# Kernel tuning notes

Measured on AMD Instinct MI355X. Metric: run time of the kernel, lower is better.

Reference implementation:

```python
import jax, jax.numpy as jnp
import numpy as np


def _encode(tab, idx):
    # tab: [F, V, D]; idx: [..., F] int -> sum_f tab[f, idx[..., f]] -> [..., D]
    g = jax.vmap(lambda t, i: t[i], in_axes=(0, -1), out_axes=0)(tab, idx)
    return g.sum(0)


def _diffuse(fea, ei, w, order):
    # fea: [N, D]; ei: [2, E]; w: [E] learned edge weights
    N = fea.shape[0]
    r, c = ei[0], ei[1]
    adj = jnp.zeros((N, N), fea.dtype).at[r, c].set(w).at[c, r].set(w)
    adj = adj + jnp.eye(N, dtype=fea.dtype)
    r_col_inv = adj.sum(1) ** -0.5  # from degree over axis 1
    r_row_inv = adj.sum(0) ** -0.5  # from degree over axis 0
    A = r_row_inv[:, None] * adj * r_col_inv[None, :]
    x = fea
    y = fea
    for _ in range(order):
        x = jax.lax.stop_gradient(A @ x)
        y = y + x
    return jax.lax.stop_gradient(y / (order + 1.0))


def setup_inputs():
    B, N, E, EMB, L, FA, FB, V = 512, 128, 512, 300, 5, 9, 3, 64
    k = jax.random.split(jax.random.key(0), 12)
    s = 0.02
    return {
        "order": 3,
        "x_atom": jax.random.randint(k[0], (B, N, FA), 0, V),
        "edge_index": jax.random.randint(k[1], (B, 2, E), 0, N),
        "edge_attr": jax.random.randint(k[2], (B, E, FB), 0, V),
        "atom_tab": jax.random.normal(k[3], (FA, V, EMB)) * s,
        "bond_tab_root": jax.random.normal(k[4], (FB, V, EMB)) * s,
        "edge_lin_w": jax.random.normal(k[5], (EMB,)) * s,
        "edge_lin_b": jnp.zeros(()),
        "bond_tabs": jax.random.normal(k[6], (L, FB, V, EMB)) * s,
        "eps": jnp.zeros((L,)),
        "w1": jax.random.normal(k[7], (L, EMB, 2 * EMB)) * s,
        "b1": jnp.zeros((L, 2 * EMB)),
        "bn1_g": jnp.ones((L, 2 * EMB)),
        "bn1_b": jnp.zeros((L, 2 * EMB)),
        "w2": jax.random.normal(k[8], (L, 2 * EMB, EMB)) * s,
        "b2": jnp.zeros((L, EMB)),
        "bn_g": jnp.ones((L, EMB)),
        "bn_b": jnp.zeros((L, EMB)),
    }


def reference(order, x_atom, edge_index, edge_attr, atom_tab, bond_tab_root,
              edge_lin_w, edge_lin_b, bond_tabs, eps, w1, b1, bn1_g, bn1_b,
              w2, b2, bn_g, bn_b):
    B, N = x_atom.shape[:2]
    E = edge_index.shape[-1]
    L = w1.shape[0]
    DROP = 0.2  # node-feature drop rate (eval-mode scaling)

    # --- per-graph dense-adjacency diffusion (vmapped over graphs) ---
    fea = _encode(atom_tab, x_atom) * (1.0 - DROP)                 # [B, N, D]
    e_emb = _encode(bond_tab_root, edge_attr)                      # [B, E, D]
    ew = jax.nn.sigmoid(e_emb @ edge_lin_w + edge_lin_b)           # [B, E]
    h = jax.vmap(_diffuse, in_axes=(0, 0, 0, None))(fea, edge_index, ew, order)
    h = h.reshape(B * N, -1)                                       # [B*N, D]

    # --- globally-batched GIN message passing ---
    off = (jnp.arange(B) * N)[:, None]
    src = (edge_index[:, 0, :] + off).reshape(-1)                  # [B*E]
    dst = (edge_index[:, 1, :] + off).reshape(-1)
    ea_flat = edge_attr.reshape(B * E, -1)

    for l in range(L):
        ee = _encode(bond_tabs[l], ea_flat)                        # [B*E, D]
        msg = jax.nn.relu(h[src] + ee)
        agg = jax.ops.segment_sum(msg, dst, num_segments=B * N)
        z = (1.0 + eps[l]) * h + agg
        z = z @ w1[l] + b1[l]
        z = bn1_g[l] * z + bn1_b[l]   # eval-mode BN (running mean 0, var 1)
        z = jax.nn.relu(z)
        z = z @ w2[l] + b2[l]
        z = bn_g[l] * z + bn_b[l]     # outer eval-mode BN
        if l < L - 1:
            z = jax.nn.relu(z)
        h = z
    return h
```

## Files before the change

kernel.cpp:

```cpp
#include <hip/hip_runtime.h>

#define NGRAPH 512
#define NNODE  128
#define NEDGE  512
#define EMB    300
#define NLAYER 5
#define FA     9
#define FB     3
#define VV     64
#define KPAD   136

typedef __bf16 bf16x8 __attribute__((ext_vector_type(8)));
typedef __bf16 bf16x4 __attribute__((ext_vector_type(4)));
typedef float  f32x4  __attribute__((ext_vector_type(4)));

__device__ __forceinline__ void gload_lds16(const void* gptr, void* lptr) {
    __builtin_amdgcn_global_load_lds(
        (const __attribute__((address_space(1))) void*)gptr,
        (__attribute__((address_space(3))) void*)lptr, 16, 0, 0);
}

__global__ __launch_bounds__(256)
void prep_w_kernel(const float* __restrict__ w1, const float* __restrict__ w2,
                   __bf16* __restrict__ w1t, __bf16* __restrict__ w2t)
{
    const int i = blockIdx.x * 256 + threadIdx.x;
    const int T1 = NLAYER * 640 * 320;
    const int T2 = NLAYER * 320 * 640;
    if (i < T1) {
        const int l = i / (640 * 320);
        const int r = i - l * 640 * 320;
        const int n = r / 320, k = r - n * 320;
        float v = (n < 600 && k < 300) ? w1[((size_t)l * 300 + k) * 600 + n] : 0.f;
        w1t[i] = (__bf16)v;
    } else if (i < T1 + T2) {
        const int j = i - T1;
        const int l = j / (320 * 640);
        const int r = j - l * 320 * 640;
        const int n = r / 640, k = r - n * 640;
        float v = (n < 300 && k < 600) ? w2[((size_t)l * 600 + k) * 300 + n] : 0.f;
        w2t[j] = (__bf16)v;
    }
}

__global__ __launch_bounds__(128)
void csr_kernel(const int* __restrict__ edge_index,
                const int* __restrict__ edge_attr,
                int* __restrict__ epk_sorted,
                int* __restrict__ off_g)
{
    __shared__ int epk_s[NEDGE];
    __shared__ int cnt[128];
    __shared__ int off_[129];

    const int tid = threadIdx.x;
    const int g   = blockIdx.x;

    cnt[tid] = 0;
    __syncthreads();
    for (int e = tid; e < NEDGE; e += 128) {
        const int s_ = edge_index[(g * 2 + 0) * NEDGE + e];
        const int d_ = edge_index[(g * 2 + 1) * NEDGE + e];
        const int base = (g * NEDGE + e) * 3;
        epk_s[e] = s_ | (d_ << 7) | (edge_attr[base + 0] << 14)
                 | (edge_attr[base + 1] << 20) | (edge_attr[base + 2] << 26);
        atomicAdd(&cnt[d_], 1);
    }
    __syncthreads();
    if (tid < 64) {
        const int a = cnt[tid];
        const int b = cnt[64 + tid];
        int ia = a;
        #pragma unroll
        for (int o = 1; o < 64; o <<= 1) {
            int t = __shfl_up(ia, o, 64);
            if (tid >= o) ia += t;
        }
        const int totA = __shfl(ia, 63, 64);
        int ib = b;
        #pragma unroll
        for (int o = 1; o < 64; o <<= 1) {
            int t = __shfl_up(ib, o, 64);
            if (tid >= o) ib += t;
        }
        off_[tid]      = ia - a;
        off_[64 + tid] = totA + ib - b;
        if (tid == 63) off_[128] = totA + ib;
    }
    __syncthreads();
    off_g[g * 129 + tid] = off_[tid];
    if (tid == 0) off_g[g * 129 + 128] = off_[128];
    int pos = off_[tid];
    for (int e = 0; e < NEDGE; ++e) {
        const int p = epk_s[e];
        if (((p >> 7) & 127) == tid) epk_sorted[(g << 9) + pos++] = p;
    }
}

__global__ __launch_bounds__(512)
void adj_kernel(const int* __restrict__ edge_index,
                const int* __restrict__ edge_attr,
                const float* __restrict__ bond_tab_root,
                const float* __restrict__ edge_lin_w,
                const float* __restrict__ edge_lin_b,
                __bf16* __restrict__ Ahi_g, __bf16* __restrict__ Alo_g)
{
    __shared__ float A[128 * 129];
    __shared__ float ew_s[NEDGE];
    __shared__ int   es[NEDGE];
    __shared__ float rinv[128];
    __shared__ float cinv[128];

    const int tid = threadIdx.x;
    const int g   = blockIdx.x;
    int* Ai = (int*)A;

    for (int e = tid; e < NEDGE; e += 512) {
        int r = edge_index[(g * 2 + 0) * NEDGE + e];
        int c = edge_index[(g * 2 + 1) * NEDGE + e];
        es[e] = r | (c << 8);
    }
    for (int i = tid; i < 128 * 129; i += 512) Ai[i] = -1;
    __syncthreads();

    {
        const int wave = tid >> 6, lane = tid & 63;
        const int sub = lane >> 3, sl = lane & 7;
        const float elb = edge_lin_b[0];
        #pragma unroll 2
        for (int it = 0; it < 8; ++it) {
            const int e = wave * 64 + it * 8 + sub;
            const int base = (g * NEDGE + e) * 3;
            const int a0 = edge_attr[base + 0];
            const int a1 = edge_attr[base + 1];
            const int a2 = edge_attr[base + 2];
            const float* t0 = bond_tab_root + (0 * VV + a0) * EMB;
            const float* t1 = bond_tab_root + (1 * VV + a1) * EMB;
            const float* t2 = bond_tab_root + (2 * VV + a2) * EMB;
            float acc = 0.f;
            for (int d = sl; d < EMB; d += 8)
                acc += (t0[d] + t1[d] + t2[d]) * edge_lin_w[d];
            acc += __shfl_xor(acc, 4, 64);
            acc += __shfl_xor(acc, 2, 64);
            acc += __shfl_xor(acc, 1, 64);
            if (sl == 0) ew_s[e] = 1.f / (1.f + expf(-(acc + elb)));
        }
    }
    for (int e = tid; e < NEDGE; e += 512) {
        int r = es[e] & 255, c = es[e] >> 8;
        atomicMax(&Ai[r * 129 + c], e);
        atomicMax(&Ai[c * 129 + r], 512 + e);
    }
    __syncthreads();
    for (int i = tid; i < 128 * 129; i += 512) {
        int p = Ai[i];
        A[i] = (p < 0) ? 0.f : ew_s[p & 511];
    }
    __syncthreads();
    if (tid < 128) A[tid * 129 + tid] += 1.f;
    __syncthreads();
    if (tid < 128) {
        float rs = 0.f, cs = 0.f;
        for (int j = 0; j < 128; ++j) { rs += A[tid * 129 + j]; cs += A[j * 129 + tid]; }
        rinv[tid] = 1.f / sqrtf(rs);
        cinv[tid] = 1.f / sqrtf(cs);
    }
    __syncthreads();
    for (int i = tid; i < 128 * KPAD; i += 512) {
        const int m = i / KPAD, k = i - m * KPAD;
        float v = (k < 128) ? A[m * 129 + k] * cinv[m] * rinv[k] : 0.f;
        __bf16 hi = (__bf16)v;
        Ahi_g[(size_t)g * 128 * KPAD + i] = hi;
        Alo_g[(size_t)g * 128 * KPAD + i] = (__bf16)(v - (float)hi);
    }
}

__global__ __launch_bounds__(1024)
void diffuse_mm_kernel(const int* __restrict__ order_p,
                       const int* __restrict__ x_atom,
                       const float* __restrict__ atom_tab,
                       const __bf16* __restrict__ Ahi_g,
                       const __bf16* __restrict__ Alo_g,
                       __bf16* __restrict__ hb)
{
    __shared__ __bf16 Ahi[128 * KPAD];
    __shared__ __bf16 Alo[128 * KPAD];
    __shared__ __bf16 xt[2 * 64 * KPAD];
    __shared__ int    xat[128 * FA];

    const int tid  = threadIdx.x;
    const int g    = blockIdx.x;
    const int lane = tid & 63;
    const int wid  = tid >> 6;
    const int wm   = (wid >> 2) * 32;
    const int wn   = (wid & 3) * 16;
    const int lr   = lane & 15;
    const int q4   = (lane >> 4) * 4;
    const int kc   = (lane >> 4) * 8;

    for (int idx = tid; idx < 128 * KPAD / 8; idx += 1024) {
        gload_lds16(Ahi_g + (size_t)g * 128 * KPAD + idx * 8, (char*)Ahi + idx * 16);
        gload_lds16(Alo_g + (size_t)g * 128 * KPAD + idx * 8, (char*)Alo + idx * 16);
    }
    for (int i = tid; i < 128 * FA; i += 1024) xat[i] = x_atom[g * 128 * FA + i];
    __syncthreads();

    const int   ord    = order_p[0];
    const float yscale = 1.f / (float)(ord + 1);
    const int   n_     = wn + lr;

    for (int cb = 0; cb < 5; ++cb) {
        const int dbase = cb * 64;
        const int d     = dbase + n_;

        float yacc[2][4];
        #pragma unroll
        for (int mi = 0; mi < 2; ++mi) {
            #pragma unroll
            for (int r = 0; r < 4; ++r) {
                const int m_ = wm + mi * 16 + q4 + r;
                float v = 0.f;
                if (d < EMB) {
                    #pragma unroll
                    for (int f = 0; f < FA; ++f)
                        v += atom_tab[(size_t)((f << 6) + xat[m_ * FA + f]) * EMB + d];
                    v *= 0.8f;
                }
                yacc[mi][r] = v;
                xt[0 * 64 * KPAD + n_ * KPAD + m_] = (__bf16)v;
            }
        }
        __syncthreads();

        int curbuf = 0;
        for (int o = 0; o < ord; ++o) {
            const __bf16* xh = xt + curbuf * 64 * KPAD;
            f32x4 racc[2];
            racc[0] = (f32x4){0.f, 0.f, 0.f, 0.f};
            racc[1] = (f32x4){0.f, 0.f, 0.f, 0.f};

            #pragma unroll
            for (int ks = 0; ks < 4; ++ks) {
                const int k0 = ks * 32 + kc;
                bf16x8 ah[2], al[2], bh;
                #pragma unroll
                for (int mi = 0; mi < 2; ++mi) {
                    ah[mi] = *(const bf16x8*)&Ahi[(wm + mi * 16 + lr) * KPAD + k0];
                    al[mi] = *(const bf16x8*)&Alo[(wm + mi * 16 + lr) * KPAD + k0];
                }
                bh = *(const bf16x8*)&xh[(wn + lr) * KPAD + k0];
                #pragma unroll
                for (int mi = 0; mi < 2; ++mi) {
                    racc[mi] = __builtin_amdgcn_mfma_f32_16x16x32_bf16(
                        ah[mi], bh, racc[mi], 0, 0, 0);
                    racc[mi] = __builtin_amdgcn_mfma_f32_16x16x32_bf16(
                        al[mi], bh, racc[mi], 0, 0, 0);
                }
            }

            __bf16* nh = xt + (curbuf ^ 1) * 64 * KPAD;
            #pragma unroll
            for (int mi = 0; mi < 2; ++mi) {
                const int mbase = wm + mi * 16 + q4;
                bf16x4 hv;
                #pragma unroll
                for (int r = 0; r < 4; ++r) {
                    const float v = racc[mi][r];
                    yacc[mi][r] += v;
                    hv[r] = (__bf16)v;
                }
                *(bf16x4*)&nh[n_ * KPAD + mbase] = hv;
            }
            __syncthreads();
            curbuf ^= 1;
        }

        #pragma unroll
        for (int mi = 0; mi < 2; ++mi) {
            #pragma unroll
            for (int r = 0; r < 4; ++r) {
                const int m_ = wm + mi * 16 + q4 + r;
                const float v = (d < EMB) ? yacc[mi][r] * yscale : 0.f;
                hb[(size_t)(g * 128 + m_) * 320 + d] = (__bf16)v;
            }
        }
    }
}

__global__ __launch_bounds__(1024)
void agg_kernel(const __bf16* __restrict__ hb,
                const int* __restrict__ epk_sorted,
                const int* __restrict__ off_g,
                const float* __restrict__ bond_tabs,
                const float* __restrict__ eps_all,
                const int l,
                __bf16* __restrict__ zb)
{
    __shared__ __bf16 hs[128 * 160];

    const int tid  = threadIdx.x;
    const int g    = blockIdx.x >> 1;
    const int coff = (blockIdx.x & 1) * 160;
    const int wave = tid >> 6, lane = tid & 63;
    const float epl = 1.f + eps_all[l];
    const float* bt = bond_tabs + (size_t)l * FB * VV * EMB;

    for (int idx = tid; idx < 128 * 20; idx += 1024) {
        const int r = idx / 20, c = idx - r * 20;
        *(bf16x8*)&hs[r * 160 + c * 8] =
            *(const bf16x8*)&hb[(size_t)(g * 128 + r) * 320 + coff + c * 8];
    }
    __syncthreads();

    const int d0 = lane, d1 = lane + 64, d2 = lane + 128;
    const bool r0 = (coff + d0) < EMB;
    const bool r1 = (coff + d1) < EMB;
    const bool r2 = (d2 < 160) && ((coff + d2) < EMB);

    const int* offg = off_g + g * 129;
    const int* epkg = epk_sorted + (g << 9);

    for (int n = wave; n < 128; n += 16) {
        float a0 = r0 ? epl * (float)hs[n * 160 + d0] : 0.f;
        float a1 = r1 ? epl * (float)hs[n * 160 + d1] : 0.f;
        float a2 = r2 ? epl * (float)hs[n * 160 + d2] : 0.f;
        const int eBeg = offg[n], eEnd = offg[n + 1];
        for (int ee = eBeg; ee < eEnd; ++ee) {
            const int p   = epkg[ee];
            const int src = p & 127;
            const float* t0 = bt + ((p >> 14) & 63) * EMB + coff;
            const float* t1 = bt + (64  + ((p >> 20) & 63)) * EMB + coff;
            const float* t2 = bt + (128 + ((p >> 26) & 63)) * EMB + coff;
            if (r0) a0 += fmaxf((float)hs[src * 160 + d0] + t0[d0] + t1[d0] + t2[d0], 0.f);
            if (r1) a1 += fmaxf((float)hs[src * 160 + d1] + t0[d1] + t1[d1] + t2[d1], 0.f);
            if (r2) a2 += fmaxf((float)hs[src * 160 + d2] + t0[d2] + t1[d2] + t2[d2], 0.f);
        }
        __bf16* zrow = zb + (size_t)(g * 128 + n) * 320 + coff;
        zrow[d0] = (__bf16)a0;
        zrow[d1] = (__bf16)a1;
        if (d2 < 160) zrow[d2] = (__bf16)a2;
    }
}

template <int CBF16, int RELU>
__global__ __launch_bounds__(256)
void gemm_mfma(const __bf16* __restrict__ A, const int lda,
               const int nT, const int nBlkN, const __bf16* __restrict__ B,
               void* __restrict__ Cv, const int ldc, const int Nreal,
               const float* __restrict__ bias, const float* __restrict__ gam,
               const float* __restrict__ bet)
{
    __shared__ __align__(16) char smem_raw[12288];
    unsigned short* As = (unsigned short*)smem_raw;
    unsigned short* Bs = (unsigned short*)(smem_raw + 8192);

    const int tid  = threadIdx.x;
    const int nwg  = gridDim.x;
    const int hw   = blockIdx.x;
    const int lg   = (hw & 7) * (nwg >> 3) + (hw >> 3);
    const int bn   = (lg % nBlkN) * 64;
    const int bm   = (lg / nBlkN) * 128;
    const int wid  = tid >> 6;
    const int lane = tid & 63;
    const int wm   = (wid >> 1) * 64;
    const int wn   = (wid & 1) * 32;
    const int lr   = lane & 15;
    const int kc   = (lane >> 4) * 8;
    const int q4   = (lane >> 4) * 4;
    const int KP   = nT * 32;

    f32x4 acc[4][2];
    #pragma unroll
    for (int mi = 0; mi < 4; ++mi)
        #pragma unroll
        for (int ni = 0; ni < 2; ++ni) acc[mi][ni] = (f32x4){0.f, 0.f, 0.f, 0.f};

    for (int t = 0; t < nT; ++t) {
        const int k0 = t * 32;
        {
            const int n = tid >> 2, k8 = (tid & 3) * 8;
            gload_lds16(B + (size_t)(bn + n) * KP + k0 + k8,
                        (char*)Bs + tid * 16);
        }
        #pragma unroll
        for (int q = 0; q < 2; ++q) {
            const int idx = q * 256 + tid;
            const int m = idx >> 2, k8 = (idx & 3) * 8;
            gload_lds16(A + (size_t)(bm + m) * lda + k0 + k8,
                        (char*)As + idx * 16);
        }
        __syncthreads();

        bf16x8 a[4], bfr[2];
        #pragma unroll
        for (int mi = 0; mi < 4; ++mi)
            a[mi] = *(const bf16x8*)&As[(wm + mi * 16 + lr) * 32 + kc];
        #pragma unroll
        for (int ni = 0; ni < 2; ++ni)
            bfr[ni] = *(const bf16x8*)&Bs[(wn + ni * 16 + lr) * 32 + kc];
        #pragma unroll
        for (int mi = 0; mi < 4; ++mi)
            #pragma unroll
            for (int ni = 0; ni < 2; ++ni)
                acc[mi][ni] = __builtin_amdgcn_mfma_f32_16x16x32_bf16(
                    a[mi], bfr[ni], acc[mi][ni], 0, 0, 0);
        __syncthreads();
    }

    float gv[2], bv[2], ev[2];
    #pragma unroll
    for (int ni = 0; ni < 2; ++ni) {
        const int n = bn + wn + ni * 16 + lr;
        const bool nv = (n < Nreal);
        gv[ni] = nv ? gam[n]  : 0.f;
        bv[ni] = nv ? bias[n] : 0.f;
        ev[ni] = nv ? bet[n]  : 0.f;
    }

    if (CBF16) {
        __bf16* Cb = (__bf16*)smem_raw;
        #pragma unroll
        for (int half = 0; half < 2; ++half) {
            if ((wm >> 6) == half) {
                #pragma unroll
                for (int ni = 0; ni < 2; ++ni) {
                    const int nl = wn + ni * 16 + lr;
                    #pragma unroll
                    for (int mi = 0; mi < 4; ++mi) {
                        #pragma unroll
                        for (int r = 0; r < 4; ++r) {
                            float v = gv[ni] * (acc[mi][ni][r] + bv[ni]) + ev[ni];
                            if (RELU) v = fmaxf(v, 0.f);
                            Cb[(mi * 16 + q4 + r) * 72 + nl] = (__bf16)v;
                        }
                    }
                }
            }
            __syncthreads();
            #pragma unroll
            for (int q = 0; q < 2; ++q) {
                const int idx = q * 256 + tid;
                const int row = idx >> 3, c16 = (idx & 7) * 8;
                const size_t m = (size_t)bm + half * 64 + row;
                *(bf16x8*)&((__bf16*)Cv)[m * ldc + bn + c16] =
                    *(const bf16x8*)&Cb[row * 72 + c16];
            }
            __syncthreads();
        }
    } else {
        float* Cf = (float*)smem_raw;
        const int ncols = (Nreal - bn < 64) ? (Nreal - bn) : 64;
        const int nch = ncols >> 2;
        #pragma unroll
        for (int mq = 0; mq < 4; ++mq) {
            if ((wm >> 6) == (mq >> 1)) {
                const int mi0 = (mq & 1) * 2;
                #pragma unroll
                for (int ni = 0; ni < 2; ++ni) {
                    const int nl = wn + ni * 16 + lr;
                    #pragma unroll
                    for (int mi2 = 0; mi2 < 2; ++mi2) {
                        const int mi = mi0 + mi2;
                        #pragma unroll
                        for (int r = 0; r < 4; ++r) {
                            float v = gv[ni] * (acc[mi][ni][r] + bv[ni]) + ev[ni];
                            if (RELU) v = fmaxf(v, 0.f);
                            Cf[(mi2 * 16 + q4 + r) * 68 + nl] = v;
                        }
                    }
                }
            }
            __syncthreads();
            for (int idx = tid; idx < 32 * nch; idx += 256) {
                const int row = idx / nch, c4 = (idx - row * nch) * 4;
                const size_t m = (size_t)bm + mq * 32 + row;
                *(float4*)&((float*)Cv)[m * ldc + bn + c4] =
                    *(const float4*)&Cf[row * 68 + c4];
            }
            __syncthreads();
        }
    }
}

extern "C" void kernel_launch(void* const* d_in, const int* in_sizes, int n_in,
                              void* d_out, int out_size, void* d_ws, size_t ws_size,
                              hipStream_t stream)
{
    const int*   order_p       = (const int*)d_in[0];
    const int*   x_atom        = (const int*)d_in[1];
    const int*   edge_index    = (const int*)d_in[2];
    const int*   edge_attr     = (const int*)d_in[3];
    const float* atom_tab      = (const float*)d_in[4];
    const float* bond_tab_root = (const float*)d_in[5];
    const float* edge_lin_w    = (const float*)d_in[6];
    const float* edge_lin_b    = (const float*)d_in[7];
    const float* bond_tabs     = (const float*)d_in[8];
    const float* eps           = (const float*)d_in[9];
    const float* w1            = (const float*)d_in[10];
    const float* b1            = (const float*)d_in[11];
    const float* bn1g          = (const float*)d_in[12];
    const float* bn1b          = (const float*)d_in[13];
    const float* w2            = (const float*)d_in[14];
    const float* b2            = (const float*)d_in[15];
    const float* bng           = (const float*)d_in[16];
    const float* bnb           = (const float*)d_in[17];

    float*  h  = (float*)d_out;
    __bf16* hb = (__bf16*)d_out;

    char* ws = (char*)d_ws;
    __bf16* Ahi_g = (__bf16*)ws;
    __bf16* Alo_g = (__bf16*)(ws + 17825792);
    __bf16* z1    = (__bf16*)ws;
    __bf16* w1t   = (__bf16*)(ws + 83886080);
    __bf16* w2t   = (__bf16*)(ws + 83886080 + 2048000);
    __bf16* zb    = (__bf16*)(ws + 83886080 + 4096000);
    int*    epk_s = (int*)(ws + 83886080 + 4096000 + 41943040);
    int*    off_g = (int*)(ws + 83886080 + 4096000 + 41943040 + 1048576);

    prep_w_kernel<<<8000, 256, 0, stream>>>(w1, w2, w1t, w2t);

    csr_kernel<<<NGRAPH, 128, 0, stream>>>(edge_index, edge_attr, epk_s, off_g);

    adj_kernel<<<NGRAPH, 512, 0, stream>>>(edge_index, edge_attr, bond_tab_root,
                                           edge_lin_w, edge_lin_b, Ahi_g, Alo_g);

    diffuse_mm_kernel<<<NGRAPH, 1024, 0, stream>>>(order_p, x_atom, atom_tab,
                                                   Ahi_g, Alo_g, hb);

    for (int l = 0; l < NLAYER; ++l) {
        agg_kernel<<<NGRAPH * 2, 1024, 0, stream>>>(
            hb, epk_s, off_g, bond_tabs, eps, l, zb);

        gemm_mfma<1, 1><<<5120, 256, 0, stream>>>(
            zb, 320, 10, 10, w1t + (size_t)l * 640 * 320,
            z1, 640, 600, b1 + l * 600, bn1g + l * 600, bn1b + l * 600);

        if (l < NLAYER - 1) {
            gemm_mfma<1, 1><<<2560, 256, 0, stream>>>(
                z1, 640, 20, 5, w2t + (size_t)l * 320 * 640,
                hb, 320, 300, b2 + l * 300, bng + l * 300, bnb + l * 300);
        } else {
            gemm_mfma<0, 0><<<2560, 256, 0, stream>>>(
                z1, 640, 20, 5, w2t + (size_t)l * 320 * 640,
                h, EMB, 300, b2 + l * 300, bng + l * 300, bnb + l * 300);
        }
    }
}
```

Baseline: 1.057 ms.

## Stage full-K weight tile in LDS and stream A fragments directly from global

```diff
diff --git a/kernel.cpp b/kernel.cpp
--- a/kernel.cpp
+++ b/kernel.cpp
@@ -342,17 +342,15 @@
     }
 }
 
-template <int CBF16, int RELU>
+template <int NCH, int CBF16, int RELU>
 __global__ __launch_bounds__(256)
-void gemm_mfma(const __bf16* __restrict__ A, const int lda,
-               const int nT, const int nBlkN, const __bf16* __restrict__ B,
-               void* __restrict__ Cv, const int ldc, const int Nreal,
-               const float* __restrict__ bias, const float* __restrict__ gam,
-               const float* __restrict__ bet)
-{
-    __shared__ __align__(16) char smem_raw[12288];
-    unsigned short* As = (unsigned short*)smem_raw;
-    unsigned short* Bs = (unsigned short*)(smem_raw + 8192);
+void gemm_skinny(const __bf16* __restrict__ A, const int lda,
+                 const int nBlkN, const __bf16* __restrict__ B,
+                 void* __restrict__ Cv, const int ldc, const int Nreal,
+                 const float* __restrict__ bias, const float* __restrict__ gam,
+                 const float* __restrict__ bet)
+{
+    __shared__ __align__(16) char smem_raw[64 * 328 * 2];
 
     const int tid  = threadIdx.x;
     const int nwg  = gridDim.x;
@@ -367,7 +365,9 @@
     const int lr   = lane & 15;
     const int kc   = (lane >> 4) * 8;
     const int q4   = (lane >> 4) * 4;
-    const int KP   = nT * 32;
+    const int KPg  = NCH * 320;
+
+    unsigned short* Bs = (unsigned short*)smem_raw;
 
     f32x4 acc[4][2];
     #pragma unroll
@@ -375,37 +375,38 @@
         #pragma unroll
         for (int ni = 0; ni < 2; ++ni) acc[mi][ni] = (f32x4){0.f, 0.f, 0.f, 0.f};
 
-    for (int t = 0; t < nT; ++t) {
-        const int k0 = t * 32;
-        {
-            const int n = tid >> 2, k8 = (tid & 3) * 8;
-            gload_lds16(B + (size_t)(bn + n) * KP + k0 + k8,
-                        (char*)Bs + tid * 16);
-        }
-        #pragma unroll
-        for (int q = 0; q < 2; ++q) {
+    #pragma unroll
+    for (int ch = 0; ch < NCH; ++ch) {
+        if (ch > 0) __syncthreads();
+        #pragma unroll
+        for (int q = 0; q < 10; ++q) {
             const int idx = q * 256 + tid;
-            const int m = idx >> 2, k8 = (idx & 3) * 8;
-            gload_lds16(A + (size_t)(bm + m) * lda + k0 + k8,
-                        (char*)As + idx * 16);
+            const int row = idx / 40, c8 = (idx - row * 40) * 8;
+            bf16x8 v = *(const bf16x8*)&B[(size_t)(bn + row) * KPg + ch * 320 + c8];
+            *(bf16x8*)&Bs[row * 328 + c8] = v;
         }
         __syncthreads();
 
-        bf16x8 a[4], bfr[2];
-        #pragma unroll
-        for (int mi = 0; mi < 4; ++mi)
-            a[mi] = *(const bf16x8*)&As[(wm + mi * 16 + lr) * 32 + kc];
-        #pragma unroll
-        for (int ni = 0; ni < 2; ++ni)
-            bfr[ni] = *(const bf16x8*)&Bs[(wn + ni * 16 + lr) * 32 + kc];
-        #pragma unroll
-        for (int mi = 0; mi < 4; ++mi)
+        const __bf16* Abase = A + (size_t)bm * lda + ch * 320;
+        #pragma unroll
+        for (int kt = 0; kt < 10; ++kt) {
+            const int k0 = kt * 32 + kc;
+            bf16x8 a[4], b[2];
+            #pragma unroll
+            for (int mi = 0; mi < 4; ++mi)
+                a[mi] = *(const bf16x8*)&Abase[(size_t)(wm + mi * 16 + lr) * lda + k0];
             #pragma unroll
             for (int ni = 0; ni < 2; ++ni)
-                acc[mi][ni] = __builtin_amdgcn_mfma_f32_16x16x32_bf16(
-                    a[mi], bfr[ni], acc[mi][ni], 0, 0, 0);
-        __syncthreads();
-    }
+                b[ni] = *(const bf16x8*)&Bs[(wn + ni * 16 + lr) * 328 + k0];
+            #pragma unroll
+            for (int mi = 0; mi < 4; ++mi)
+                #pragma unroll
+                for (int ni = 0; ni < 2; ++ni)
+                    acc[mi][ni] = __builtin_amdgcn_mfma_f32_16x16x32_bf16(
+                        a[mi], b[ni], acc[mi][ni], 0, 0, 0);
+        }
+    }
+    __syncthreads();
 
     float gv[2], bv[2], ev[2];
     #pragma unroll
@@ -532,17 +533,17 @@
         agg_kernel<<<NGRAPH * 2, 1024, 0, stream>>>(
             hb, epk_s, off_g, bond_tabs, eps, l, zb);
 
-        gemm_mfma<1, 1><<<5120, 256, 0, stream>>>(
-            zb, 320, 10, 10, w1t + (size_t)l * 640 * 320,
+        gemm_skinny<1, 1, 1><<<5120, 256, 0, stream>>>(
+            zb, 320, 10, w1t + (size_t)l * 640 * 320,
             z1, 640, 600, b1 + l * 600, bn1g + l * 600, bn1b + l * 600);
 
         if (l < NLAYER - 1) {
-            gemm_mfma<1, 1><<<2560, 256, 0, stream>>>(
-                z1, 640, 20, 5, w2t + (size_t)l * 320 * 640,
+            gemm_skinny<2, 1, 1><<<2560, 256, 0, stream>>>(
+                z1, 640, 5, w2t + (size_t)l * 320 * 640,
                 hb, 320, 300, b2 + l * 300, bng + l * 300, bnb + l * 300);
         } else {
-            gemm_mfma<0, 0><<<2560, 256, 0, stream>>>(
-                z1, 640, 20, 5, w2t + (size_t)l * 320 * 640,
+            gemm_skinny<2, 0, 0><<<2560, 256, 0, stream>>>(
+                z1, 640, 5, w2t + (size_t)l * 320 * 640,
                 h, EMB, 300, b2 + l * 300, bng + l * 300, bnb + l * 300);
         }
     }
```

Result: slower. 1.637 ms (+54.8%).

## Process two feature chunks concurrently in diffusion and interleave two nodes in aggregation

Applied to the files above, without the earlier changes.

```diff
diff --git a/kernel.cpp b/kernel.cpp
--- a/kernel.cpp
+++ b/kernel.cpp
@@ -185,15 +185,17 @@
 {
     __shared__ __bf16 Ahi[128 * KPAD];
     __shared__ __bf16 Alo[128 * KPAD];
-    __shared__ __bf16 xt[2 * 64 * KPAD];
+    __shared__ __bf16 xt[4 * 64 * KPAD];
     __shared__ int    xat[128 * FA];
 
     const int tid  = threadIdx.x;
     const int g    = blockIdx.x;
     const int lane = tid & 63;
     const int wid  = tid >> 6;
-    const int wm   = (wid >> 2) * 32;
-    const int wn   = (wid & 3) * 16;
+    const int cs   = wid >> 3;
+    const int w8   = wid & 7;
+    const int wm   = (w8 >> 1) * 32;
+    const int wn   = (w8 & 1) * 32;
     const int lr   = lane & 15;
     const int q4   = (lane >> 4) * 4;
     const int kc   = (lane >> 4) * 8;
@@ -207,81 +209,104 @@
 
     const int   ord    = order_p[0];
     const float yscale = 1.f / (float)(ord + 1);
-    const int   n_     = wn + lr;
-
-    for (int cb = 0; cb < 5; ++cb) {
-        const int dbase = cb * 64;
-        const int d     = dbase + n_;
-
-        float yacc[2][4];
+
+    for (int cb = 0; cb < 3; ++cb) {
+        const int  chunk = cb * 2 + cs;
+        const bool valid = (chunk < 5);
+        const int  dbase = chunk * 64;
+
+        float yacc[2][2][4];
         #pragma unroll
         for (int mi = 0; mi < 2; ++mi) {
             #pragma unroll
-            for (int r = 0; r < 4; ++r) {
-                const int m_ = wm + mi * 16 + q4 + r;
-                float v = 0.f;
-                if (d < EMB) {
-                    #pragma unroll
-                    for (int f = 0; f < FA; ++f)
-                        v += atom_tab[(size_t)((f << 6) + xat[m_ * FA + f]) * EMB + d];
-                    v *= 0.8f;
+            for (int ni = 0; ni < 2; ++ni) {
+                const int n_ = wn + ni * 16 + lr;
+                const int d  = dbase + n_;
+                #pragma unroll
+                for (int r = 0; r < 4; ++r) {
+                    const int m_ = wm + mi * 16 + q4 + r;
+                    float v = 0.f;
+                    if (valid && d < EMB) {
+                        #pragma unroll
+                        for (int f = 0; f < FA; ++f)
+                            v += atom_tab[(size_t)((f << 6) + xat[m_ * FA + f]) * EMB + d];
+                        v *= 0.8f;
+                    }
+                    yacc[mi][ni][r] = v;
+                    xt[(cs * 2 + 0) * 64 * KPAD + n_ * KPAD + m_] = (__bf16)v;
                 }
-                yacc[mi][r] = v;
-                xt[0 * 64 * KPAD + n_ * KPAD + m_] = (__bf16)v;
             }
         }
         __syncthreads();
 
         int curbuf = 0;
         for (int o = 0; o < ord; ++o) {
-            const __bf16* xh = xt + curbuf * 64 * KPAD;
-            f32x4 racc[2];
-            racc[0] = (f32x4){0.f, 0.f, 0.f, 0.f};
-            racc[1] = (f32x4){0.f, 0.f, 0.f, 0.f};
+            const __bf16* xh = xt + (cs * 2 + curbuf) * 64 * KPAD;
+            f32x4 racc[2][2];
+            #pragma unroll
+            for (int mi = 0; mi < 2; ++mi)
+                #pragma unroll
+                for (int ni = 0; ni < 2; ++ni) racc[mi][ni] = (f32x4){0.f, 0.f, 0.f, 0.f};
 
             #pragma unroll
             for (int ks = 0; ks < 4; ++ks) {
                 const int k0 = ks * 32 + kc;
-                bf16x8 ah[2], al[2], bh;
+                bf16x8 ah[2], al[2], bh[2];
                 #pragma unroll
                 for (int mi = 0; mi < 2; ++mi) {
                     ah[mi] = *(const bf16x8*)&Ahi[(wm + mi * 16 + lr) * KPAD + k0];
                     al[mi] = *(const bf16x8*)&Alo[(wm + mi * 16 + lr) * KPAD + k0];
                 }
-                bh = *(const bf16x8*)&xh[(wn + lr) * KPAD + k0];
+                #pragma unroll
+                for (int ni = 0; ni < 2; ++ni)
+                    bh[ni] = *(const bf16x8*)&xh[(wn + ni * 16 + lr) * KPAD + k0];
                 #pragma unroll
                 for (int mi = 0; mi < 2; ++mi) {
-                    racc[mi] = __builtin_amdgcn_mfma_f32_16x16x32_bf16(
-                        ah[mi], bh, racc[mi], 0, 0, 0);
-                    racc[mi] = __builtin_amdgcn_mfma_f32_16x16x32_bf16(
-                        al[mi], bh, racc[mi], 0, 0, 0);
+                    #pragma unroll
+                    for (int ni = 0; ni < 2; ++ni) {
+                        racc[mi][ni] = __builtin_amdgcn_mfma_f32_16x16x32_bf16(
+                            ah[mi], bh[ni], racc[mi][ni], 0, 0, 0);
+                        racc[mi][ni] = __builtin_amdgcn_mfma_f32_16x16x32_bf16(
+                            al[mi], bh[ni], racc[mi][ni], 0, 0, 0);
+                    }
                 }
             }
 
-            __bf16* nh = xt + (curbuf ^ 1) * 64 * KPAD;
+            __bf16* nh = xt + (cs * 2 + (curbuf ^ 1)) * 64 * KPAD;
             #pragma unroll
             for (int mi = 0; mi < 2; ++mi) {
-                const int mbase = wm + mi * 16 + q4;
-                bf16x4 hv;
-                #pragma unroll
-                for (int r = 0; r < 4; ++r) {
-                    const float v = racc[mi][r];
-                    yacc[mi][r] += v;
-                    hv[r] = (__bf16)v;
+                #pragma unroll
+                for (int ni = 0; ni < 2; ++ni) {
+                    const int n_ = wn + ni * 16 + lr;
+                    const int mbase = wm + mi * 16 + q4;
+                    bf16x4 hv;
+                    #pragma unroll
+                    for (int r = 0; r < 4; ++r) {
+                        const float v = racc[mi][ni][r];
+                        yacc[mi][ni][r] += v;
+                        hv[r] = (__bf16)v;
+                    }
+                    *(bf16x4*)&nh[n_ * KPAD + mbase] = hv;
                 }
-                *(bf16x4*)&nh[n_ * KPAD + mbase] = hv;
             }
             __syncthreads();
             curbuf ^= 1;
         }
 
-        #pragma unroll
-        for (int mi = 0; mi < 2; ++mi) {
+        if (valid) {
             #pragma unroll
-            for (int r = 0; r < 4; ++r) {
-                const int m_ = wm + mi * 16 + q4 + r;
-                const float v = (d < EMB) ? yacc[mi][r] * yscale : 0.f;
-                hb[(size_t)(g * 128 + m_) * 320 + d] = (__bf16)v;
+            for (int mi = 0; mi < 2; ++mi) {
+                #pragma unroll
+                for (int ni = 0; ni < 2; ++ni) {
+                    const int n_ = wn + ni * 16 + lr;
+                    const int d  = dbase + n_;
+                    #pragma unroll
+                    for (int r = 0; r < 4; ++r) {
+                        const int m_ = wm + mi * 16 + q4 + r;
+                        const float v = (d < EMB) ? yacc[mi][ni][r] * yscale : 0.f;
+                        hb[(size_t)(g * 128 + m_) * 320 + d] = (__bf16)v;
+                    }
+                }
             }
         }
     }
@@ -320,13 +345,43 @@
     const int* offg = off_g + g * 129;
     const int* epkg = epk_sorted + (g << 9);
 
-    for (int n = wave; n < 128; n += 16) {
-        float a0 = r0 ? epl * (float)hs[n * 160 + d0] : 0.f;
-        float a1 = r1 ? epl * (float)hs[n * 160 + d1] : 0.f;
-        float a2 = r2 ? epl * (float)hs[n * 160 + d2] : 0.f;
-        const int eBeg = offg[n], eEnd = offg[n + 1];
-        for (int ee = eBeg; ee < eEnd; ++ee) {
-            const int p   = epkg[ee];
+    for (int nb = wave; nb < 64; nb += 16) {
+        const int n0 = nb, n1 = nb + 64;
+        float a0 = r0 ? epl * (float)hs[n0 * 160 + d0] : 0.f;
+        float a1 = r1 ? epl * (float)hs[n0 * 160 + d1] : 0.f;
+        float a2 = r2 ? epl * (float)hs[n0 * 160 + d2] : 0.f;
+        float b0 = r0 ? epl * (float)hs[n1 * 160 + d0] : 0.f;
+        float b1 = r1 ? epl * (float)hs[n1 * 160 + d1] : 0.f;
+        float b2 = r2 ? epl * (float)hs[n1 * 160 + d2] : 0.f;
+        int eA = offg[n0];
+        int eB = offg[n1];
+        const int eAe = offg[n0 + 1];
+        const int eBe = offg[n1 + 1];
+
+        while (eA < eAe && eB < eBe) {
+            {
+                const int p   = epkg[eA++];
+                const int src = p & 127;
+                const float* t0 = bt + ((p >> 14) & 63) * EMB + coff;
+                const float* t1 = bt + (64  + ((p >> 20) & 63)) * EMB + coff;
+                const float* t2 = bt + (128 + ((p >> 26) & 63)) * EMB + coff;
+                if (r0) a0 += fmaxf((float)hs[src * 160 + d0] + t0[d0] + t1[d0] + t2[d0], 0.f);
+                if (r1) a1 += fmaxf((float)hs[src * 160 + d1] + t0[d1] + t1[d1] + t2[d1], 0.f);
+                if (r2) a2 += fmaxf((float)hs[src * 160 + d2] + t0[d2] + t1[d2] + t2[d2], 0.f);
+            }
+            {
+                const int p   = epkg[eB++];
+                const int src = p & 127;
+                const float* t0 = bt + ((p >> 14) & 63) * EMB + coff;
+                const float* t1 = bt + (64  + ((p >> 20) & 63)) * EMB + coff;
+                const float* t2 = bt + (128 + ((p >> 26) & 63)) * EMB + coff;
+                if (r0) b0 += fmaxf((float)hs[src * 160 + d0] + t0[d0] + t1[d0] + t2[d0], 0.f);
+                if (r1) b1 += fmaxf((float)hs[src * 160 + d1] + t0[d1] + t1[d1] + t2[d1], 0.f);
+                if (r2) b2 += fmaxf((float)hs[src * 160 + d2] + t0[d2] + t1[d2] + t2[d2], 0.f);
+            }
+        }
+        while (eA < eAe) {
+            const int p   = epkg[eA++];
             const int src = p & 127;
             const float* t0 = bt + ((p >> 14) & 63) * EMB + coff;
             const float* t1 = bt + (64  + ((p >> 20) & 63)) * EMB + coff;
@@ -335,10 +390,25 @@
             if (r1) a1 += fmaxf((float)hs[src * 160 + d1] + t0[d1] + t1[d1] + t2[d1], 0.f);
             if (r2) a2 += fmaxf((float)hs[src * 160 + d2] + t0[d2] + t1[d2] + t2[d2], 0.f);
         }
-        __bf16* zrow = zb + (size_t)(g * 128 + n) * 320 + coff;
-        zrow[d0] = (__bf16)a0;
-        zrow[d1] = (__bf16)a1;
-        if (d2 < 160) zrow[d2] = (__bf16)a2;
+        while (eB < eBe) {
+            const int p   = epkg[eB++];
+            const int src = p & 127;
+            const float* t0 = bt + ((p >> 14) & 63) * EMB + coff;
+            const float* t1 = bt + (64  + ((p >> 20) & 63)) * EMB + coff;
+            const float* t2 = bt + (128 + ((p >> 26) & 63)) * EMB + coff;
+            if (r0) b0 += fmaxf((float)hs[src * 160 + d0] + t0[d0] + t1[d0] + t2[d0], 0.f);
+            if (r1) b1 += fmaxf((float)hs[src * 160 + d1] + t0[d1] + t1[d1] + t2[d1], 0.f);
+            if (r2) b2 += fmaxf((float)hs[src * 160 + d2] + t0[d2] + t1[d2] + t2[d2], 0.f);
+        }
+
+        __bf16* zr0 = zb + (size_t)(g * 128 + n0) * 320 + coff;
+        __bf16* zr1 = zb + (size_t)(g * 128 + n1) * 320 + coff;
+        zr0[d0] = (__bf16)a0;
+        zr0[d1] = (__bf16)a1;
+        if (d2 < 160) zr0[d2] = (__bf16)a2;
+        zr1[d0] = (__bf16)b0;
+        zr1[d1] = (__bf16)b1;
+        if (d2 < 160) zr1[d2] = (__bf16)b2;
     }
 }
 
```

Result: no change. 1.068 ms, median of 2 (+1.0%).
